# Optimization experiments

Measured on AMD Instinct MI355X. Metric: run time of the kernel, lower is better.

Reference implementation:

```python
import jax, jax.numpy as jnp
import numpy as np
from jax import lax

B = 32768
IMG = 28
K = 3
OUT_HW = IMG - K + 1  # 26
FLAT = OUT_HW * OUT_HW  # 676
HID = 300
NCLS = 10


def setup_inputs() -> dict:
    key = jax.random.key(0)
    ks = jax.random.split(key, 8)
    x = jax.random.normal(ks[0], (B, IMG * IMG), dtype=jnp.float32)
    conv_w = jax.random.normal(ks[1], (K, K), dtype=jnp.float32) * 0.1
    # Linear params stored as (in, out) so forward is h @ W + b
    W1 = jax.random.normal(ks[2], (FLAT, HID), dtype=jnp.float32) * 0.04
    b1 = jnp.zeros((HID,), dtype=jnp.float32)
    W2 = jax.random.normal(ks[3], (HID, HID), dtype=jnp.float32) * 0.06
    b2 = jnp.zeros((HID,), dtype=jnp.float32)
    W3 = jax.random.normal(ks[4], (HID, NCLS), dtype=jnp.float32) * 0.06
    b3 = jnp.zeros((NCLS,), dtype=jnp.float32)
    return {"x": x, "conv_w": conv_w, "W1": W1, "b1": b1,
            "W2": W2, "b2": b2, "W3": W3, "b3": b3}


def reference(x, conv_w, W1, b1, W2, b2, W3, b3):
    b = x.shape[0]
    img = x.reshape(b, 1, IMG, IMG)  # NCHW
    # Valid cross-correlation with 3x3 kernel -> [B,1,26,26]
    y = lax.conv_general_dilated(
        img, conv_w[None, None, :, :], window_strides=(1, 1), padding="VALID",
        dimension_numbers=("NCHW", "OIHW", "NCHW"))
    h = y.reshape(b, FLAT)
    h = jax.nn.relu(h @ W1 + b1)
    h = jax.nn.relu(h @ W2 + b2)
    return h @ W3 + b3
```

## Files before the change

### kernel.cpp

```cpp
#include <hip/hip_runtime.h>


typedef __bf16 bf16_t;
typedef __bf16 bf16x8 __attribute__((ext_vector_type(8)));
typedef float  f32x4  __attribute__((ext_vector_type(4)));

#define MFMA16(a, b, c) __builtin_amdgcn_mfma_f32_16x16x32_bf16((a), (b), (c), 0, 0, 0)

#define W1F_ELEMS (25 * 20 * 64 * 8)
#define W2F_ELEMS (10 * 20 * 64 * 8)
#define W3F_ELEMS (10 * 1 * 64 * 8)

#define XSLOT 16384
#define XBASE 40960

__global__ void prep_weights(const float* __restrict__ conv_w,
                             const float* __restrict__ W1,
                             const float* __restrict__ W2,
                             const float* __restrict__ W3,
                             bf16_t* __restrict__ W1f,
                             bf16_t* __restrict__ W2f,
                             bf16_t* __restrict__ W3f) {
    int idx = blockIdx.x * 256 + threadIdx.x;
    if (idx < 800 * 320) {
        int k = idx / 320;
        int n = idx - k * 320;
        float v = 0.0f;
        if (k < 784 && n < 300) {
            int py = k / 28;
            int px = k - py * 28;
#pragma unroll
            for (int ky = 0; ky < 3; ++ky) {
                int oy = py - ky;
                if (oy < 0 || oy > 25) continue;
#pragma unroll
                for (int kx = 0; kx < 3; ++kx) {
                    int ox = px - kx;
                    if (ox < 0 || ox > 25) continue;
                    v += conv_w[ky * 3 + kx] * W1[(oy * 26 + ox) * 300 + n];
                }
            }
        }
        int kc = k >> 5, quad = (k >> 3) & 3, j = k & 7;
        int nt = n >> 4, nin = n & 15;
        W1f[(((kc * 20 + nt) * 64 + quad * 16 + nin) << 3) + j] = (bf16_t)v;
    } else if (idx < 800 * 320 + 320 * 320) {
        int i2 = idx - 800 * 320;
        int k = i2 / 320;
        int n = i2 - k * 320;
        float v = (k < 300 && n < 300) ? W2[k * 300 + n] : 0.0f;
        int kc = k >> 5, quad = (k >> 3) & 3, j = k & 7;
        int nt = n >> 4, nin = n & 15;
        W2f[(((kc * 20 + nt) * 64 + quad * 16 + nin) << 3) + j] = (bf16_t)v;
    } else if (idx < 800 * 320 + 320 * 320 + 320 * 16) {
        int i3 = idx - (800 * 320 + 320 * 320);
        int k = i3 / 16;
        int n = i3 - k * 16;
        float v = (k < 300 && n < 10) ? W3[k * 10 + n] : 0.0f;
        int kc = k >> 5, quad = (k >> 3) & 3, j = k & 7;
        W3f[(((kc * 64) + quad * 16 + n) << 3) + j] = (bf16_t)v;
    }
}

__device__ __forceinline__ void stage16(const void* g, void* l) {
    __builtin_amdgcn_global_load_lds(
        (const __attribute__((address_space(1))) void*)g,
        (__attribute__((address_space(3))) void*)l, 16, 0, 0);
}

__global__ __launch_bounds__(512, 4) void fused_mlp(
    const float* __restrict__ x, const float* __restrict__ b1,
    const float* __restrict__ b2, const float* __restrict__ b3,
    const bf16x8* __restrict__ W1f, const bf16x8* __restrict__ W2f,
    const bf16x8* __restrict__ W3f, float* __restrict__ out) {
    __shared__ __align__(16) unsigned char smem[XBASE + 2 * XSLOT];
    bf16x8* Bb   = (bf16x8*)smem;
    bf16x8* hbuf = (bf16x8*)smem;
    bf16_t* hb   = (bf16_t*)smem;

    const int tid = threadIdx.x;
    const int w   = tid >> 6;
    const int l   = tid & 63;
    const int q   = l >> 4;
    const int l15 = l & 15;
    const int r0  = blockIdx.x * 64;

    const bool t3    = (w < 4);
    const int  nt0   = t3 ? (w * 3) : (12 + (w - 4) * 2);
    const int  boff2 = t3 ? 128 : 64;

    f32x4 acc[4][3];
#pragma unroll
    for (int m = 0; m < 4; ++m)
#pragma unroll
        for (int j = 0; j < 3; ++j) acc[m][j] = (f32x4){0.f, 0.f, 0.f, 0.f};

#define STAGE_B(KC, BUF)                                                       \
    {                                                                          \
        const bf16x8* ws_ = W1f + (size_t)(KC)*1280 + l;                       \
        bf16x8* wd_ = Bb + (BUF)*1280;                                         \
        stage16(ws_ + w * 64, wd_ + w * 64);                                   \
        stage16(ws_ + (w + 8) * 64, wd_ + (w + 8) * 64);                       \
        if (w >= 4) stage16(ws_ + (w + 12) * 64, wd_ + (w + 12) * 64);         \
    }

#define STAGE_BAND(BAND)                                                       \
    {                                                                          \
        unsigned char* slot_ = smem + XBASE + ((BAND)&1) * XSLOT;              \
        if ((BAND) < 12) {                                                     \
            _Pragma("unroll")                                                  \
            for (int i_ = 0; i_ < 2; ++i_) {                                   \
                int row_ = w * 8 + i_ * 4 + (l >> 4);                          \
                int u_   = (l & 15) ^ (row_ & 7);                              \
                stage16(x + (size_t)(r0 + row_) * 784 + (BAND)*64 + u_ * 4,    \
                        slot_ + w * 2048 + i_ * 1024);                         \
            }                                                                  \
        } else {                                                               \
            int row_ = w * 8 + (l >> 3);                                       \
            int u_   = (l & 7) ^ (row_ & 7);                                   \
            const float* src_ = x + (size_t)(r0 + row_) * 784 +                \
                                ((u_ < 4) ? (768 + u_ * 4) : 0);               \
            stage16(src_, slot_ + w * 1024);                                   \
        }                                                                      \
    }

#define AFRAG(DST, SLOT, RS, KCL, MT)                                          \
    {                                                                          \
        int row_ = (MT)*16 + l15;                                              \
        int r7_  = row_ & 7;                                                   \
        float4 fa_ = *(const float4*)((SLOT) + row_ * (RS) +                   \
                     ((((KCL)*8 + q * 2 + 0) ^ r7_) << 4));                    \
        float4 fb_ = *(const float4*)((SLOT) + row_ * (RS) +                   \
                     ((((KCL)*8 + q * 2 + 1) ^ r7_) << 4));                    \
        bf16x8 t_;                                                             \
        t_[0] = (bf16_t)fa_.x; t_[1] = (bf16_t)fa_.y;                          \
        t_[2] = (bf16_t)fa_.z; t_[3] = (bf16_t)fa_.w;                          \
        t_[4] = (bf16_t)fb_.x; t_[5] = (bf16_t)fb_.y;                          \
        t_[6] = (bf16_t)fb_.z; t_[7] = (bf16_t)fb_.w;                          \
        DST = t_;                                                              \
    }

#define G1CHUNK(SLOT, RS, KCL, BUF)                                            \
    {                                                                          \
        bf16x8 a0, a1, a2, a3;                                                 \
        AFRAG(a0, SLOT, RS, KCL, 0) AFRAG(a1, SLOT, RS, KCL, 1)                \
        AFRAG(a2, SLOT, RS, KCL, 2) AFRAG(a3, SLOT, RS, KCL, 3)                \
        const bf16x8* bb_ = Bb + (BUF)*1280 + nt0 * 64 + l;                    \
        bf16x8 b0 = bb_[0], b1v = bb_[64], b2v = bb_[boff2];                   \
        acc[0][0] = MFMA16(a0, b0, acc[0][0]);                                 \
        acc[1][0] = MFMA16(a1, b0, acc[1][0]);                                 \
        acc[2][0] = MFMA16(a2, b0, acc[2][0]);                                 \
        acc[3][0] = MFMA16(a3, b0, acc[3][0]);                                 \
        acc[0][1] = MFMA16(a0, b1v, acc[0][1]);                                \
        acc[1][1] = MFMA16(a1, b1v, acc[1][1]);                                \
        acc[2][1] = MFMA16(a2, b1v, acc[2][1]);                                \
        acc[3][1] = MFMA16(a3, b1v, acc[3][1]);                                \
        if (t3) {                                                              \
            acc[0][2] = MFMA16(a0, b2v, acc[0][2]);                            \
            acc[1][2] = MFMA16(a1, b2v, acc[1][2]);                            \
            acc[2][2] = MFMA16(a2, b2v, acc[2][2]);                            \
            acc[3][2] = MFMA16(a3, b2v, acc[3][2]);                            \
        }                                                                      \
    }

#define VMW(N) asm volatile("s_waitcnt vmcnt(" #N ") lgkmcnt(0)" ::: "memory")
#define BARRIER()                         \
    __builtin_amdgcn_s_barrier();         \
    __builtin_amdgcn_sched_barrier(0)

    STAGE_B(0, 0)
    STAGE_BAND(0)
    VMW(0);
    BARRIER();

    for (int b = 0; b <= 10; ++b) {
        unsigned char* xs = smem + XBASE + (b & 1) * XSLOT;
        const int k0 = 2 * b;
        STAGE_B(k0 + 1, (k0 + 1) & 1)
        STAGE_BAND(b + 1)
        G1CHUNK(xs, 256, 0, k0 & 1)
        VMW(2);
        BARRIER();
        STAGE_B(k0 + 2, (k0 + 2) & 1)
        G1CHUNK(xs, 256, 1, (k0 + 1) & 1)
        VMW(0);
        BARRIER();
    }
    {
        unsigned char* xs = smem + XBASE + XSLOT;
        STAGE_B(23, 1)
        STAGE_BAND(12)
        G1CHUNK(xs, 256, 0, 0)
        VMW(1);
        BARRIER();
        STAGE_B(24, 0)
        G1CHUNK(xs, 256, 1, 1)
        VMW(0);
        BARRIER();
    }
    {
        unsigned char* xs = smem + XBASE;
        G1CHUNK(xs, 128, 0, 0)
        asm volatile("s_waitcnt lgkmcnt(0)" ::: "memory");
        BARRIER();
    }

#define HSTORE(J, BIAS)                                                        \
    {                                                                          \
        int n = (nt0 + (J)) * 16 + l15;                                        \
        float bias = (n < 300) ? (BIAS)[n] : 0.0f;                             \
        int kh = n >> 5, quad = (n >> 3) & 3, jj = n & 7;                      \
        _Pragma("unroll")                                                      \
        for (int mt = 0; mt < 4; ++mt)                                         \
            _Pragma("unroll")                                                  \
            for (int r = 0; r < 4; ++r) {                                      \
                float v = acc[mt][(J)][r] + bias;                              \
                v = v > 0.f ? v : 0.f;                                         \
                hb[(((kh * 4 + mt) * 64 + quad * 16 + q * 4 + r) << 3) + jj] = \
                    (bf16_t)v;                                                 \
            }                                                                  \
    }

    HSTORE(0, b1)
    HSTORE(1, b1)
    if (t3) HSTORE(2, b1)
    asm volatile("s_waitcnt lgkmcnt(0)" ::: "memory");
    BARRIER();

#pragma unroll
    for (int m = 0; m < 4; ++m)
#pragma unroll
        for (int j = 0; j < 3; ++j) acc[m][j] = (f32x4){0.f, 0.f, 0.f, 0.f};

    const bf16x8* bB2 = W2f + nt0 * 64 + l;

#define G2CHUNK(KC2)                                                           \
    {                                                                          \
        bf16x8 a0 = hbuf[((KC2)*4 + 0) * 64 + l];                              \
        bf16x8 a1 = hbuf[((KC2)*4 + 1) * 64 + l];                              \
        bf16x8 a2 = hbuf[((KC2)*4 + 2) * 64 + l];                              \
        bf16x8 a3 = hbuf[((KC2)*4 + 3) * 64 + l];                              \
        const bf16x8* bp = bB2 + (KC2)*1280;                                   \
        bf16x8 b0 = bp[0], b1v = bp[64], b2v = bp[boff2];                      \
        acc[0][0] = MFMA16(a0, b0, acc[0][0]);                                 \
        acc[1][0] = MFMA16(a1, b0, acc[1][0]);                                 \
        acc[2][0] = MFMA16(a2, b0, acc[2][0]);                                 \
        acc[3][0] = MFMA16(a3, b0, acc[3][0]);                                 \
        acc[0][1] = MFMA16(a0, b1v, acc[0][1]);                                \
        acc[1][1] = MFMA16(a1, b1v, acc[1][1]);                                \
        acc[2][1] = MFMA16(a2, b1v, acc[2][1]);                                \
        acc[3][1] = MFMA16(a3, b1v, acc[3][1]);                                \
        if (t3) {                                                              \
            acc[0][2] = MFMA16(a0, b2v, acc[0][2]);                            \
            acc[1][2] = MFMA16(a1, b2v, acc[1][2]);                            \
            acc[2][2] = MFMA16(a2, b2v, acc[2][2]);                            \
            acc[3][2] = MFMA16(a3, b2v, acc[3][2]);                            \
        }                                                                      \
    }

    G2CHUNK(0) G2CHUNK(1) G2CHUNK(2) G2CHUNK(3) G2CHUNK(4)
    G2CHUNK(5) G2CHUNK(6) G2CHUNK(7) G2CHUNK(8) G2CHUNK(9)

    asm volatile("s_waitcnt lgkmcnt(0)" ::: "memory");
    BARRIER();

    HSTORE(0, b2)
    HSTORE(1, b2)
    if (t3) HSTORE(2, b2)
    asm volatile("s_waitcnt lgkmcnt(0)" ::: "memory");
    BARRIER();

    if (w < 4) {
        f32x4 acc3 = (f32x4){0.f, 0.f, 0.f, 0.f};
#pragma unroll
        for (int kc3 = 0; kc3 < 10; ++kc3)
            acc3 = MFMA16(hbuf[(kc3 * 4 + w) * 64 + l], W3f[kc3 * 64 + l], acc3);
        if (l15 < 10) {
            float bias = b3[l15];
#pragma unroll
            for (int r = 0; r < 4; ++r)
                out[(size_t)(r0 + w * 16 + q * 4 + r) * 10 + l15] = acc3[r] + bias;
        }
    }
}

extern "C" void kernel_launch(void* const* d_in, const int* in_sizes, int n_in,
                              void* d_out, int out_size, void* d_ws, size_t ws_size,
                              hipStream_t stream) {
    const float* x      = (const float*)d_in[0];
    const float* conv_w = (const float*)d_in[1];
    const float* W1     = (const float*)d_in[2];
    const float* b1     = (const float*)d_in[3];
    const float* W2     = (const float*)d_in[4];
    const float* b2     = (const float*)d_in[5];
    const float* W3     = (const float*)d_in[6];
    const float* b3     = (const float*)d_in[7];
    float* out = (float*)d_out;

    char* ws = (char*)d_ws;
    bf16_t* W1f = (bf16_t*)(ws);
    bf16_t* W2f = (bf16_t*)(ws + (size_t)W1F_ELEMS * 2);
    bf16_t* W3f = (bf16_t*)(ws + (size_t)(W1F_ELEMS + W2F_ELEMS) * 2);
    if (ws_size < (size_t)(W1F_ELEMS + W2F_ELEMS + W3F_ELEMS) * 2) return;

    int prep_total = 800 * 320 + 320 * 320 + 320 * 16;
    prep_weights<<<(prep_total + 255) / 256, 256, 0, stream>>>(
        conv_w, W1, W2, W3, W1f, W2f, W3f);

    fused_mlp<<<32768 / 64, 512, 0, stream>>>(
        x, b1, b2, b3, (const bf16x8*)W1f, (const bf16x8*)W2f,
        (const bf16x8*)W3f, out);
}
```

Baseline: 181.2 us.

## Split fused MLP into separate layer-1 and tail kernels via global intermediate

The single fused kernel is split in two. The first computes conv+layer1 and writes the bf16 hidden activations to workspace. The second reads them straight from global memory as MFMA A operands, then runs layer 2 and layer 3. This likely aims to cut shared memory per block in the tail and to isolate the stages, but it adds a global round trip for the 64-row hidden tile, a second launch, and uncached global A-operand loads.

```diff
diff --git a/kernel.cpp b/kernel.cpp
--- a/kernel.cpp
+++ b/kernel.cpp
@@ -10,6 +10,7 @@
 #define W1F_ELEMS (25 * 20 * 64 * 8)
 #define W2F_ELEMS (10 * 20 * 64 * 8)
 #define W3F_ELEMS (10 * 1 * 64 * 8)
+#define H1F_GRPS  (512 * 2560)
 
 #define XSLOT 16384
 #define XBASE 40960
@@ -68,11 +69,15 @@
         (__attribute__((address_space(3))) void*)l, 16, 0, 0);
 }
 
-__global__ __launch_bounds__(512, 4) void fused_mlp(
+#define VMW(N) asm volatile("s_waitcnt vmcnt(" #N ") lgkmcnt(0)" ::: "memory")
+#define LGKM0() asm volatile("s_waitcnt lgkmcnt(0)" ::: "memory")
+#define BARRIER()                         \
+    __builtin_amdgcn_s_barrier();         \
+    __builtin_amdgcn_sched_barrier(0)
+
+__global__ __launch_bounds__(512, 4) void gemm1_k(
     const float* __restrict__ x, const float* __restrict__ b1,
-    const float* __restrict__ b2, const float* __restrict__ b3,
-    const bf16x8* __restrict__ W1f, const bf16x8* __restrict__ W2f,
-    const bf16x8* __restrict__ W3f, float* __restrict__ out) {
+    const bf16x8* __restrict__ W1f, bf16x8* __restrict__ h1f) {
     __shared__ __align__(16) unsigned char smem[XBASE + 2 * XSLOT];
     bf16x8* Bb   = (bf16x8*)smem;
     bf16x8* hbuf = (bf16x8*)smem;
@@ -163,11 +168,6 @@
         }                                                                      \
     }
 
-#define VMW(N) asm volatile("s_waitcnt vmcnt(" #N ") lgkmcnt(0)" ::: "memory")
-#define BARRIER()                         \
-    __builtin_amdgcn_s_barrier();         \
-    __builtin_amdgcn_sched_barrier(0)
-
     STAGE_B(0, 0)
     STAGE_BAND(0)
     VMW(0);
@@ -201,7 +201,7 @@
     {
         unsigned char* xs = smem + XBASE;
         G1CHUNK(xs, 128, 0, 0)
-        asm volatile("s_waitcnt lgkmcnt(0)" ::: "memory");
+        LGKM0();
         BARRIER();
     }
 
@@ -224,22 +224,50 @@
     HSTORE(0, b1)
     HSTORE(1, b1)
     if (t3) HSTORE(2, b1)
-    asm volatile("s_waitcnt lgkmcnt(0)" ::: "memory");
+    LGKM0();
     BARRIER();
 
+    bf16x8* hg = h1f + (size_t)blockIdx.x * 2560;
+#pragma unroll
+    for (int i = 0; i < 5; ++i) {
+        int t = i * 512 + tid;
+        hg[t] = hbuf[t];
+    }
+}
+
+__global__ __launch_bounds__(512, 4) void tail_k(
+    const bf16x8* __restrict__ h1f, const float* __restrict__ b2,
+    const float* __restrict__ b3, const bf16x8* __restrict__ W2f,
+    const bf16x8* __restrict__ W3f, float* __restrict__ out) {
+    __shared__ __align__(16) bf16x8 hbuf[2560];
+    bf16_t* hb = (bf16_t*)hbuf;
+
+    const int tid = threadIdx.x;
+    const int w   = tid >> 6;
+    const int l   = tid & 63;
+    const int q   = l >> 4;
+    const int l15 = l & 15;
+    const int r0  = blockIdx.x * 64;
+
+    const bool t3    = (w < 4);
+    const int  nt0   = t3 ? (w * 3) : (12 + (w - 4) * 2);
+    const int  boff2 = t3 ? 128 : 64;
+
+    f32x4 acc[4][3];
 #pragma unroll
     for (int m = 0; m < 4; ++m)
 #pragma unroll
         for (int j = 0; j < 3; ++j) acc[m][j] = (f32x4){0.f, 0.f, 0.f, 0.f};
 
+    const bf16x8* hg  = h1f + (size_t)blockIdx.x * 2560;
     const bf16x8* bB2 = W2f + nt0 * 64 + l;
 
-#define G2CHUNK(KC2)                                                           \
-    {                                                                          \
-        bf16x8 a0 = hbuf[((KC2)*4 + 0) * 64 + l];                              \
-        bf16x8 a1 = hbuf[((KC2)*4 + 1) * 64 + l];                              \
-        bf16x8 a2 = hbuf[((KC2)*4 + 2) * 64 + l];                              \
-        bf16x8 a3 = hbuf[((KC2)*4 + 3) * 64 + l];                              \
+#define G2CHUNKG(KC2)                                                          \
+    {                                                                          \
+        bf16x8 a0 = hg[((KC2)*4 + 0) * 64 + l];                                \
+        bf16x8 a1 = hg[((KC2)*4 + 1) * 64 + l];                                \
+        bf16x8 a2 = hg[((KC2)*4 + 2) * 64 + l];                                \
+        bf16x8 a3 = hg[((KC2)*4 + 3) * 64 + l];                                \
         const bf16x8* bp = bB2 + (KC2)*1280;                                   \
         bf16x8 b0 = bp[0], b1v = bp[64], b2v = bp[boff2];                      \
         acc[0][0] = MFMA16(a0, b0, acc[0][0]);                                 \
@@ -258,16 +286,13 @@
         }                                                                      \
     }
 
-    G2CHUNK(0) G2CHUNK(1) G2CHUNK(2) G2CHUNK(3) G2CHUNK(4)
-    G2CHUNK(5) G2CHUNK(6) G2CHUNK(7) G2CHUNK(8) G2CHUNK(9)
-
-    asm volatile("s_waitcnt lgkmcnt(0)" ::: "memory");
-    BARRIER();
+    G2CHUNKG(0) G2CHUNKG(1) G2CHUNKG(2) G2CHUNKG(3) G2CHUNKG(4)
+    G2CHUNKG(5) G2CHUNKG(6) G2CHUNKG(7) G2CHUNKG(8) G2CHUNKG(9)
 
     HSTORE(0, b2)
     HSTORE(1, b2)
     if (t3) HSTORE(2, b2)
-    asm volatile("s_waitcnt lgkmcnt(0)" ::: "memory");
+    LGKM0();
     BARRIER();
 
     if (w < 4) {
@@ -301,13 +326,16 @@
     bf16_t* W1f = (bf16_t*)(ws);
     bf16_t* W2f = (bf16_t*)(ws + (size_t)W1F_ELEMS * 2);
     bf16_t* W3f = (bf16_t*)(ws + (size_t)(W1F_ELEMS + W2F_ELEMS) * 2);
-    if (ws_size < (size_t)(W1F_ELEMS + W2F_ELEMS + W3F_ELEMS) * 2) return;
+    bf16x8* h1f = (bf16x8*)(ws + (((size_t)(W1F_ELEMS + W2F_ELEMS + W3F_ELEMS) * 2 + 255) & ~(size_t)255));
+    size_t need = (((size_t)(W1F_ELEMS + W2F_ELEMS + W3F_ELEMS) * 2 + 255) & ~(size_t)255) +
+                  (size_t)H1F_GRPS * 16;
+    if (ws_size < need) return;
 
     int prep_total = 800 * 320 + 320 * 320 + 320 * 16;
     prep_weights<<<(prep_total + 255) / 256, 256, 0, stream>>>(
         conv_w, W1, W2, W3, W1f, W2f, W3f);
 
-    fused_mlp<<<32768 / 64, 512, 0, stream>>>(
-        x, b1, b2, b3, (const bf16x8*)W1f, (const bf16x8*)W2f,
-        (const bf16x8*)W3f, out);
-}
+    gemm1_k<<<512, 512, 0, stream>>>(x, b1, (const bf16x8*)W1f, h1f);
+    tail_k<<<512, 512, 0, stream>>>((const bf16x8*)h1f, b2, b3,
+                                    (const bf16x8*)W2f, (const bf16x8*)W3f, out);
+}
```

Result: slower. 190.2 us (+5.0%).
